# Performance work log

Hardware: AMD Instinct MI355X
Metric: run time of the kernel (lower is better)

The kernel has to match this reference:

```python
import jax, jax.numpy as jnp
import numpy as np

E4M3_MAX = 448.0  # fp8_max_fwd for Format.HYBRID fprop tensors
MARGIN = 0        # DelayedScaling default


def _quantize_e4m3(t, s):
    # cast_to_fp8: scale, saturate-cast to E4M3; amax of the unscaled tensor
    q = (t * s).astype(jnp.float8_e4m3fn)
    amax = jnp.max(jnp.abs(t))
    return q, amax


def _sf_compute(amax, scale, fp8_max, margin):
    # faithful port of _default_sf_compute (including its tf.where ordering)
    exp = jnp.floor(jnp.log2(fp8_max / amax)) - margin
    sf = jnp.round(jnp.exp2(jnp.abs(exp)))
    sf = jnp.where(amax > 0.0, sf, scale)
    sf = jnp.where(jnp.isinf(amax), sf, scale)
    sf = jnp.where(exp < 0, 1.0 / sf, sf)
    return sf


def setup_inputs() -> dict:
    key = jax.random.key(0)
    k1, k2 = jax.random.split(key)
    M, K, N = 16384, 2048, 2048
    x = jax.random.normal(k1, (M, K), dtype=jnp.float32)
    kernel = jax.random.normal(k2, (K, N), dtype=jnp.float32) * 0.02
    scale = jnp.ones((2,), dtype=jnp.float32)
    scale_inv = jnp.ones((2,), dtype=jnp.float32)
    amax_history = jnp.zeros((1, 2), dtype=jnp.float32)
    return {"x": x, "kernel": kernel, "scale": scale,
            "scale_inv": scale_inv, "amax_history": amax_history}


def reference(x, kernel, scale, scale_inv, amax_history):
    # --- cast_to_fp8 for activation (index 0) and weight (index 1) ---
    x_q, amax_x = _quantize_e4m3(x, scale[0])          # [M, K] fp8
    w_q, amax_w = _quantize_e4m3(kernel.T, scale[1])   # [N, K] fp8 (B in row-major, gemm does B^T)
    new_scale_inv = jnp.stack([1.0 / scale[0], 1.0 / scale[1]])
    # record amaxes into most-recent slot of the history
    amax_history = amax_history.at[0, 0].set(amax_x).at[0, 1].set(amax_w)

    # --- fp8_matmul: D = (A * A_scale_inv) @ (B * B_scale_inv)^T ---
    out = jnp.matmul(x_q.astype(jnp.float32), w_q.astype(jnp.float32).T)
    out = out * (new_scale_inv[0] * new_scale_inv[1])  # [M, N]

    # --- fused_amax_and_scale_update (amax_compute_algo='most_recent') ---
    amax = amax_history[0]
    rolled = jnp.roll(amax_history, -1, axis=0).at[0].set(0.0)
    new_scale = _sf_compute(amax, scale, E4M3_MAX, MARGIN)
    return out, new_scale, rolled
```

## Files before the change

kernel.cpp:

```cpp
#include <hip/hip_runtime.h>
#include <cstdint>

#define M_DIM 16384
#define K_DIM 2048
#define N_DIM 2048

typedef float f32x4 __attribute__((ext_vector_type(4)));
typedef int   i32x8 __attribute__((ext_vector_type(8)));

__global__ __launch_bounds__(256) void quant_x_kernel(
    const float4* __restrict__ x, uint4* __restrict__ xq,
    const float* __restrict__ scale, unsigned int* __restrict__ amax)
{
    const int gid = blockIdx.x * 256 + threadIdx.x;
    const float s = scale[0];
    float m = 0.0f;
#pragma unroll
    for (int j = 0; j < 8; ++j) {
        float4 v = x[gid + j * 1048576];
        m = fmaxf(m, fmaxf(fmaxf(fabsf(v.x), fabsf(v.y)),
                           fmaxf(fabsf(v.z), fabsf(v.w))));
        unsigned int p0 = __builtin_amdgcn_cvt_pk_fp8_f32(v.x * s, v.y * s, 0, false);
        unsigned int p  = __builtin_amdgcn_cvt_pk_fp8_f32(v.z * s, v.w * s, p0, true);
        ((unsigned int*)xq)[gid + j * 1048576] = p;
    }

#pragma unroll
    for (int off = 32; off > 0; off >>= 1)
        m = fmaxf(m, __shfl_down(m, off, 64));
    __shared__ float red[4];
    if ((threadIdx.x & 63) == 0) red[threadIdx.x >> 6] = m;
    __syncthreads();
    if (threadIdx.x == 0) {
        m = fmaxf(fmaxf(red[0], red[1]), fmaxf(red[2], red[3]));
        atomicMax(amax, __float_as_uint(m));
    }
}

__global__ __launch_bounds__(256) void quant_w_kernel(
    const float* __restrict__ w, uint8_t* __restrict__ wq,
    const float* __restrict__ scale, unsigned int* __restrict__ amax)
{
    __shared__ float tile[64][68];
    const int t = threadIdx.x;
    const int nb = blockIdx.x * 64;
    const int kb = blockIdx.y * 64;
    const float s = scale[1];
    float m = 0.0f;
#pragma unroll
    for (int j = 0; j < 4; ++j) {
        int f = j * 256 + t;
        int row = f >> 4;
        int c4 = f & 15;
        float4 v = *(const float4*)(w + (size_t)(kb + row) * N_DIM + nb + c4 * 4);
        m = fmaxf(m, fmaxf(fmaxf(fabsf(v.x), fabsf(v.y)),
                           fmaxf(fabsf(v.z), fabsf(v.w))));
        *(float4*)(&tile[row][c4 * 4]) = v;
    }
    __syncthreads();
    const int n = t >> 2, c = t & 3;
    unsigned int pk[4];
#pragma unroll
    for (int jj = 0; jj < 4; ++jj) {
        float f0 = tile[c * 16 + jj * 4 + 0][n] * s;
        float f1 = tile[c * 16 + jj * 4 + 1][n] * s;
        float f2 = tile[c * 16 + jj * 4 + 2][n] * s;
        float f3 = tile[c * 16 + jj * 4 + 3][n] * s;
        unsigned int p = __builtin_amdgcn_cvt_pk_fp8_f32(f0, f1, 0, false);
        pk[jj] = __builtin_amdgcn_cvt_pk_fp8_f32(f2, f3, p, true);
    }
    *(uint4*)(wq + (size_t)(nb + n) * K_DIM + kb + c * 16) = make_uint4(pk[0], pk[1], pk[2], pk[3]);

#pragma unroll
    for (int off = 32; off > 0; off >>= 1)
        m = fmaxf(m, __shfl_down(m, off, 64));
    __shared__ float red[4];
    if ((t & 63) == 0) red[t >> 6] = m;
    __syncthreads();
    if (t == 0) {
        m = fmaxf(fmaxf(red[0], red[1]), fmaxf(red[2], red[3]));
        atomicMax(amax, __float_as_uint(m));
    }
}

#define GSTRIDE 2080
__global__ __launch_bounds__(256) void gemm_fp8_kernel(
    const uint8_t* __restrict__ Aq, const uint8_t* __restrict__ Bq,
    const float* __restrict__ scale, float* __restrict__ C)
{
    __shared__ uint8_t lA[8 * GSTRIDE];
    __shared__ uint8_t lB[8 * GSTRIDE];
    const int tid  = threadIdx.x;
    const int wave = tid >> 6;
    const int lane = tid & 63;
    const int wm = wave >> 1, wn = wave & 1;
    const int q = lane >> 4, r = lane & 15;

    const int bn = blockIdx.x;
    const int bm = blockIdx.y;
    const size_t a_base = (size_t)bm * 128 * K_DIM;
    const size_t b_base = (size_t)bn * 128 * K_DIM;

    int srow[4], skoff[4], sdst[4];
#pragma unroll
    for (int j = 0; j < 4; ++j) {
        const int s  = j * 4 + wave;
        const int g  = s >> 1, hh = s & 1;
        const int fl = hh * 32 + (lane >> 1);
        srow[j]  = g * 16 + (fl & 15);
        skoff[j] = (fl >> 4) * 32 + (lane & 1) * 16;
        sdst[j]  = g * GSTRIDE + hh * 1040 + lane * 16;
    }
    const int frag_off = lane * 32 + (lane >> 5) * 16;

    f32x4 acc[4][4];
#pragma unroll
    for (int i = 0; i < 4; ++i)
#pragma unroll
        for (int j = 0; j < 4; ++j) acc[i][j] = (f32x4){0.f, 0.f, 0.f, 0.f};

    const int SONE = 0x7F7F7F7F;

    for (int kt = 0; kt < K_DIM / 128; ++kt) {
        __syncthreads();
        const size_t kg = (size_t)kt * 128;
#pragma unroll
        for (int j = 0; j < 4; ++j) {
            const uint8_t* ga = Aq + a_base + (size_t)srow[j] * K_DIM + kg + skoff[j];
            const uint8_t* gb = Bq + b_base + (size_t)srow[j] * K_DIM + kg + skoff[j];
            __builtin_amdgcn_global_load_lds(
                (const __attribute__((address_space(1))) uint32_t*)ga,
                (__attribute__((address_space(3))) uint32_t*)(lA + sdst[j]), 16, 0, 0);
            __builtin_amdgcn_global_load_lds(
                (const __attribute__((address_space(1))) uint32_t*)gb,
                (__attribute__((address_space(3))) uint32_t*)(lB + sdst[j]), 16, 0, 0);
        }
        __syncthreads();

        i32x8 a_frag[4], b_frag[4];
#pragma unroll
        for (int mi = 0; mi < 4; ++mi) {
            const uint8_t* pa = lA + (wm * 4 + mi) * GSTRIDE + frag_off;
            int4 lo = *(const int4*)pa;
            int4 hi = *(const int4*)(pa + 16);
            a_frag[mi] = (i32x8){lo.x, lo.y, lo.z, lo.w, hi.x, hi.y, hi.z, hi.w};
        }
#pragma unroll
        for (int ni = 0; ni < 4; ++ni) {
            const uint8_t* pb = lB + (wn * 4 + ni) * GSTRIDE + frag_off;
            int4 lo = *(const int4*)pb;
            int4 hi = *(const int4*)(pb + 16);
            b_frag[ni] = (i32x8){lo.x, lo.y, lo.z, lo.w, hi.x, hi.y, hi.z, hi.w};
        }
#pragma unroll
        for (int mi = 0; mi < 4; ++mi)
#pragma unroll
            for (int ni = 0; ni < 4; ++ni)
                acc[mi][ni] = __builtin_amdgcn_mfma_scale_f32_16x16x128_f8f6f4(
                    a_frag[mi], b_frag[ni], acc[mi][ni],
                    0 , 0 ,
                    0, SONE, 0, SONE);
    }

    const float sinv = (1.0f / scale[0]) * (1.0f / scale[1]);
#pragma unroll
    for (int mi = 0; mi < 4; ++mi) {
#pragma unroll
        for (int ni = 0; ni < 4; ++ni) {
            const int col  = bn * 128 + wn * 64 + ni * 16 + r;
            const int row0 = bm * 128 + wm * 64 + mi * 16 + q * 4;
#pragma unroll
            for (int rr = 0; rr < 4; ++rr)
                C[(size_t)(row0 + rr) * N_DIM + col] = acc[mi][ni][rr] * sinv;
        }
    }
}

__global__ void finalize_kernel(const float* __restrict__ scale,
                                const unsigned int* __restrict__ amax_bits,
                                float* __restrict__ out_tail)
{
    const int i = threadIdx.x;
    if (i < 2) {
        const float amax = __uint_as_float(amax_bits[i]);
        const float sc = scale[i];
        const float e = floorf(log2f(448.0f / amax));
        float sf = roundf(exp2f(fabsf(e)));
        sf = (amax > 0.0f) ? sf : sc;
        sf = isinf(amax) ? sf : sc;
        if (e < 0.0f) sf = 1.0f / sf;
        out_tail[i] = sf;
        out_tail[2 + i] = 0.0f;
    }
}

extern "C" void kernel_launch(void* const* d_in, const int* in_sizes, int n_in,
                              void* d_out, int out_size, void* d_ws, size_t ws_size,
                              hipStream_t stream)
{
    const float* x     = (const float*)d_in[0];
    const float* w     = (const float*)d_in[1];
    const float* scale = (const float*)d_in[2];

    uint8_t* ws = (uint8_t*)d_ws;
    uint8_t* xq = ws;
    uint8_t* wq = ws + (size_t)M_DIM * K_DIM;
    unsigned int* amax = (unsigned int*)(ws + (size_t)M_DIM * K_DIM + (size_t)N_DIM * K_DIM);

    hipMemsetAsync(amax, 0, 2 * sizeof(unsigned int), stream);

    quant_x_kernel<<<4096, 256, 0, stream>>>(
        (const float4*)x, (uint4*)xq, scale, amax);

    dim3 gw(N_DIM / 64, K_DIM / 64);
    quant_w_kernel<<<gw, 256, 0, stream>>>(w, wq, scale, amax + 1);

    dim3 gg(N_DIM / 128, M_DIM / 128);
    gemm_fp8_kernel<<<gg, 256, 0, stream>>>(xq, wq, scale, (float*)d_out);

    finalize_kernel<<<1, 64, 0, stream>>>(scale, amax,
                                          (float*)d_out + (size_t)M_DIM * N_DIM);
}
```

Baseline: 337.3 us.

## Rewrite FP8 GEMM with 256x256 tiles, double-buffered LDS and swizzled layout

The GEMM kernel moves from 128x128 tiles with 4 waves to 256x256 tiles with 8 waves. Each wave now holds a 128x64 accumulator. The LDS is double-buffered at 128KB of dynamic shared memory, so the next K-tile's global_load_lds is issued while MFMAs run on the current buffer, with fine-grained vmcnt waits, barriers and setprio. An XOR swizzle replaces row padding to avoid bank conflicts. This reduces global traffic per FLOP and hides load latency, at the cost of higher register pressure, lower occupancy and only 512 blocks.

```diff
diff --git a/kernel.cpp b/kernel.cpp
--- a/kernel.cpp
+++ b/kernel.cpp
@@ -83,92 +83,131 @@
     }
 }
 
-#define GSTRIDE 2080
-__global__ __launch_bounds__(256) void gemm_fp8_kernel(
+#define LDSBUF 32768
+
+__global__ __launch_bounds__(512, 2) void gemm_fp8_kernel(
     const uint8_t* __restrict__ Aq, const uint8_t* __restrict__ Bq,
     const float* __restrict__ scale, float* __restrict__ C)
 {
-    __shared__ uint8_t lA[8 * GSTRIDE];
-    __shared__ uint8_t lB[8 * GSTRIDE];
+    extern __shared__ uint8_t lds[];
+    uint8_t* const lA = lds;
+    uint8_t* const lB = lds + 2 * LDSBUF;
+
     const int tid  = threadIdx.x;
     const int wave = tid >> 6;
     const int lane = tid & 63;
-    const int wm = wave >> 1, wn = wave & 1;
+    const int wm = wave >> 2, wn = wave & 3;
     const int q = lane >> 4, r = lane & 15;
 
     const int bn = blockIdx.x;
     const int bm = blockIdx.y;
-    const size_t a_base = (size_t)bm * 128 * K_DIM;
-    const size_t b_base = (size_t)bn * 128 * K_DIM;
-
-    int srow[4], skoff[4], sdst[4];
-#pragma unroll
-    for (int j = 0; j < 4; ++j) {
-        const int s  = j * 4 + wave;
-        const int g  = s >> 1, hh = s & 1;
-        const int fl = hh * 32 + (lane >> 1);
-        srow[j]  = g * 16 + (fl & 15);
-        skoff[j] = (fl >> 4) * 32 + (lane & 1) * 16;
-        sdst[j]  = g * GSTRIDE + hh * 1040 + lane * 16;
-    }
-    const int frag_off = lane * 32 + (lane >> 5) * 16;
-
-    f32x4 acc[4][4];
-#pragma unroll
-    for (int i = 0; i < 4; ++i)
+
+    const float s0 = scale[0];
+    const float s1 = scale[1];
+    asm volatile("s_waitcnt vmcnt(0) lgkmcnt(0)" ::: "memory");
+
+    const int seg = wave & 1;
+    const int wp  = wave >> 1;
+    const int gbB = wp + ((wp >> 1) << 1);
+    const int npr = seg * 64 + lane;
+    const int nin = npr ^ ((npr >> 3) & 1);
+    const int srow = (nin >> 1) & 15;
+    const int skb  = (((nin >> 1) >> 4) << 5) + ((nin & 1) << 4);
+    const int sdst = seg * 1024 + lane * 16;
+
+    const uint8_t* aS = Aq + (size_t)(bm * 256 + srow) * K_DIM + skb;
+    const uint8_t* bS = Bq + (size_t)(bn * 256 + srow) * K_DIM + skb;
+
+#define STAGE_A(buf, kb, g)                                                          \
+    __builtin_amdgcn_global_load_lds(                                                \
+        (const __attribute__((address_space(1))) uint32_t*)(aS + (size_t)(g) * (16 * K_DIM) + (kb)), \
+        (__attribute__((address_space(3))) uint32_t*)(lA + (buf) * LDSBUF + (g) * 2048 + sdst), 16, 0, 0)
+#define STAGE_B(buf, kb, g)                                                          \
+    __builtin_amdgcn_global_load_lds(                                                \
+        (const __attribute__((address_space(1))) uint32_t*)(bS + (size_t)(g) * (16 * K_DIM) + (kb)), \
+        (__attribute__((address_space(3))) uint32_t*)(lB + (buf) * LDSBUF + (g) * 2048 + sdst), 16, 0, 0)
+
+    const int sb   = (lane >> 2) & 1;
+    const int offL = (((lane << 1) ^ sb) << 4);
+    const int offH = ((((lane << 1) + 1) ^ sb) << 4);
+
+    f32x4 acc[8][4];
+#pragma unroll
+    for (int i = 0; i < 8; ++i)
 #pragma unroll
         for (int j = 0; j < 4; ++j) acc[i][j] = (f32x4){0.f, 0.f, 0.f, 0.f};
 
+    STAGE_A(0, 0, wp);       STAGE_A(0, 0, 8 + wp);
+    STAGE_B(0, 0, gbB);      STAGE_B(0, 0, 8 + gbB);
+    STAGE_B(0, 0, 2 + gbB);  STAGE_B(0, 0, 10 + gbB);
+    STAGE_A(0, 0, 4 + wp);   STAGE_A(0, 0, 12 + wp);
+    asm volatile("s_waitcnt vmcnt(4)" ::: "memory");
+    __builtin_amdgcn_s_barrier();
+
     const int SONE = 0x7F7F7F7F;
 
-    for (int kt = 0; kt < K_DIM / 128; ++kt) {
-        __syncthreads();
-        const size_t kg = (size_t)kt * 128;
-#pragma unroll
-        for (int j = 0; j < 4; ++j) {
-            const uint8_t* ga = Aq + a_base + (size_t)srow[j] * K_DIM + kg + skoff[j];
-            const uint8_t* gb = Bq + b_base + (size_t)srow[j] * K_DIM + kg + skoff[j];
-            __builtin_amdgcn_global_load_lds(
-                (const __attribute__((address_space(1))) uint32_t*)ga,
-                (__attribute__((address_space(3))) uint32_t*)(lA + sdst[j]), 16, 0, 0);
-            __builtin_amdgcn_global_load_lds(
-                (const __attribute__((address_space(1))) uint32_t*)gb,
-                (__attribute__((address_space(3))) uint32_t*)(lB + sdst[j]), 16, 0, 0);
+#pragma unroll 2
+    for (int t = 0; t < 16; ++t) {
+        const int cur = t & 1, nxt = cur ^ 1;
+        const int kbn = ((t + 1) & 15) * 128;
+        uint8_t* const curA = lA + cur * LDSBUF;
+        uint8_t* const curB = lB + cur * LDSBUF;
+        i32x8 a_frag[4];
+#pragma unroll
+        for (int p = 0; p < 4; ++p) {
+            const int mh = p >> 1, nh = p & 1;
+            if (nh == 0) {
+#pragma unroll
+                for (int mi = 0; mi < 4; ++mi) {
+                    const uint8_t* pa = curA + (wm * 8 + mh * 4 + mi) * 2048;
+                    int4 lo = *(const int4*)(pa + offL);
+                    int4 hi = *(const int4*)(pa + offH);
+                    a_frag[mi] = (i32x8){lo.x, lo.y, lo.z, lo.w,
+                                         hi.x, hi.y, hi.z, hi.w};
+                }
+            }
+            i32x8 b_frag[2];
+#pragma unroll
+            for (int j = 0; j < 2; ++j) {
+                const uint8_t* pb = curB + (wn * 4 + nh * 2 + j) * 2048;
+                int4 lo = *(const int4*)(pb + offL);
+                int4 hi = *(const int4*)(pb + offH);
+                b_frag[j] = (i32x8){lo.x, lo.y, lo.z, lo.w,
+                                    hi.x, hi.y, hi.z, hi.w};
+            }
+            if (p == 0)      { STAGE_A(nxt, kbn, wp);       STAGE_A(nxt, kbn, 8 + wp); }
+            else if (p == 1) { STAGE_B(nxt, kbn, gbB);      STAGE_B(nxt, kbn, 8 + gbB); }
+            else if (p == 2) { STAGE_B(nxt, kbn, 2 + gbB);  STAGE_B(nxt, kbn, 10 + gbB); }
+            else             { STAGE_A(nxt, kbn, 4 + wp);   STAGE_A(nxt, kbn, 12 + wp); }
+
+            if (p != 2) asm volatile("s_waitcnt vmcnt(4)" ::: "memory");
+            __builtin_amdgcn_s_barrier();
+            asm volatile("s_waitcnt lgkmcnt(0)" ::: "memory");
+            __builtin_amdgcn_sched_barrier(0);
+            __builtin_amdgcn_s_setprio(1);
+#pragma unroll
+            for (int mi = 0; mi < 4; ++mi)
+#pragma unroll
+                for (int j = 0; j < 2; ++j)
+                    acc[mh * 4 + mi][nh * 2 + j] =
+                        __builtin_amdgcn_mfma_scale_f32_16x16x128_f8f6f4(
+                            a_frag[mi], b_frag[j], acc[mh * 4 + mi][nh * 2 + j],
+                            0 , 0 ,
+                            0, SONE, 0, SONE);
+            __builtin_amdgcn_s_setprio(0);
+            __builtin_amdgcn_s_barrier();
         }
-        __syncthreads();
-
-        i32x8 a_frag[4], b_frag[4];
-#pragma unroll
-        for (int mi = 0; mi < 4; ++mi) {
-            const uint8_t* pa = lA + (wm * 4 + mi) * GSTRIDE + frag_off;
-            int4 lo = *(const int4*)pa;
-            int4 hi = *(const int4*)(pa + 16);
-            a_frag[mi] = (i32x8){lo.x, lo.y, lo.z, lo.w, hi.x, hi.y, hi.z, hi.w};
-        }
+    }
+#undef STAGE_A
+#undef STAGE_B
+
+    const float sinv = (1.0f / s0) * (1.0f / s1);
+#pragma unroll
+    for (int mi = 0; mi < 8; ++mi) {
 #pragma unroll
         for (int ni = 0; ni < 4; ++ni) {
-            const uint8_t* pb = lB + (wn * 4 + ni) * GSTRIDE + frag_off;
-            int4 lo = *(const int4*)pb;
-            int4 hi = *(const int4*)(pb + 16);
-            b_frag[ni] = (i32x8){lo.x, lo.y, lo.z, lo.w, hi.x, hi.y, hi.z, hi.w};
-        }
-#pragma unroll
-        for (int mi = 0; mi < 4; ++mi)
-#pragma unroll
-            for (int ni = 0; ni < 4; ++ni)
-                acc[mi][ni] = __builtin_amdgcn_mfma_scale_f32_16x16x128_f8f6f4(
-                    a_frag[mi], b_frag[ni], acc[mi][ni],
-                    0 , 0 ,
-                    0, SONE, 0, SONE);
-    }
-
-    const float sinv = (1.0f / scale[0]) * (1.0f / scale[1]);
-#pragma unroll
-    for (int mi = 0; mi < 4; ++mi) {
-#pragma unroll
-        for (int ni = 0; ni < 4; ++ni) {
-            const int col  = bn * 128 + wn * 64 + ni * 16 + r;
-            const int row0 = bm * 128 + wm * 64 + mi * 16 + q * 4;
+            const int col  = bn * 256 + wn * 64 + ni * 16 + r;
+            const int row0 = bm * 256 + wm * 128 + mi * 16 + q * 4;
 #pragma unroll
             for (int rr = 0; rr < 4; ++rr)
                 C[(size_t)(row0 + rr) * N_DIM + col] = acc[mi][ni][rr] * sinv;
@@ -207,6 +246,13 @@
     uint8_t* wq = ws + (size_t)M_DIM * K_DIM;
     unsigned int* amax = (unsigned int*)(ws + (size_t)M_DIM * K_DIM + (size_t)N_DIM * K_DIM);
 
+    static int lds_opt_in = 0;
+    if (!lds_opt_in) {
+        hipFuncSetAttribute((const void*)gemm_fp8_kernel,
+                            hipFuncAttributeMaxDynamicSharedMemorySize, 131072);
+        lds_opt_in = 1;
+    }
+
     hipMemsetAsync(amax, 0, 2 * sizeof(unsigned int), stream);
 
     quant_x_kernel<<<4096, 256, 0, stream>>>(
@@ -215,8 +261,8 @@
     dim3 gw(N_DIM / 64, K_DIM / 64);
     quant_w_kernel<<<gw, 256, 0, stream>>>(w, wq, scale, amax + 1);
 
-    dim3 gg(N_DIM / 128, M_DIM / 128);
-    gemm_fp8_kernel<<<gg, 256, 0, stream>>>(xq, wq, scale, (float*)d_out);
+    dim3 gg(N_DIM / 256, M_DIM / 256);
+    gemm_fp8_kernel<<<gg, 512, 131072, stream>>>(xq, wq, scale, (float*)d_out);
 
     finalize_kernel<<<1, 64, 0, stream>>>(scale, amax,
                                           (float*)d_out + (size_t)M_DIM * N_DIM);
```

Measured after the change: 376.6 us. +11.6%, slower.
